# Kernel optimization log

Measured on AMD Instinct MI355X. Metric: run time of the kernel, lower is better.

The kernel has to match this reference:

```python
import jax, jax.numpy as jnp
import numpy as np

B, L, D = 8, 4096, 4096
E, R, K = 8, 16, 2
ALPHA = 1.0
EPS = 1e-5

def setup_inputs() -> dict:
    key = jax.random.key(0)
    ks = jax.random.split(key, 5)
    x = jax.random.normal(ks[0], (B, L, D), dtype=jnp.float32)
    gate_w = jax.random.normal(ks[1], (E, D), dtype=jnp.float32) * 0.02
    gate_b = jnp.zeros((E,), dtype=jnp.float32)
    A_w = jax.random.normal(ks[2], (E, R, D), dtype=jnp.float32) * 0.02
    B_w = jax.random.normal(ks[3], (E, D, R), dtype=jnp.float32) * 0.02
    gamma = jnp.ones((D,), dtype=jnp.float32)
    beta = jnp.zeros((D,), dtype=jnp.float32)
    return {"x": x, "gate_w": gate_w, "gate_b": gate_b, "A_w": A_w,
            "B_w": B_w, "gamma": gamma, "beta": beta}

def reference(x, gate_w, gate_b, A_w, B_w, gamma, beta):
    scale = ALPHA / R
    # pooled hidden state per sequence: [B, D]
    h = x.mean(axis=1)
    # router: gate logits -> top-k -> softmax over selected
    logits = h @ gate_w.T + gate_b                     # [B, E]
    top_vals, top_idx = jax.lax.top_k(logits, K)       # [B, K]
    w = jax.nn.softmax(top_vals, axis=-1)              # [B, K]
    # gather selected experts' LoRA factors
    A_sel = A_w[top_idx]                               # [B, K, R, D]
    B_sel = B_w[top_idx]                               # [B, K, D, R]
    z = jnp.einsum('bkrd,bd->bkr', A_sel, h)           # down-proj
    eo = jnp.einsum('bkdr,bkr->bkd', B_sel, z) * scale # up-proj
    delta = jnp.sum(w[..., None] * eo, axis=1)         # [B, D]
    # residual + LayerNorm (broadcast delta over seq dim)
    y = x + delta[:, None, :]
    mu = y.mean(axis=-1, keepdims=True)
    var = y.var(axis=-1, keepdims=True)
    return (y - mu) * jax.lax.rsqrt(var + EPS) * gamma + beta
```

## Files before the change

### kernel.cpp

```cpp
#include <hip/hip_runtime.h>

#define BB    8
#define LSEQ  4096
#define DD    4096
#define EE    8
#define RR    16
#define KK    2
#define NSLICE 128
#define LORA_SCALE (1.0f / 16.0f)
#define LN_EPS 1e-5f

typedef float f4 __attribute__((ext_vector_type(4)));

__device__ __forceinline__ float wave_sum(float v) {
#pragma unroll
    for (int off = 32; off > 0; off >>= 1)
        v += __shfl_xor(v, off, 64);
    return v;
}

__device__ __forceinline__ float dot4(f4 a, f4 b) {
    return a.x * b.x + a.y * b.y + a.z * b.z + a.w * b.w;
}

__global__ __launch_bounds__(256) void colsum_kernel(
    const f4* __restrict__ x, f4* __restrict__ partial, int rows_per_slice)
{
    const int tid = threadIdx.x;
    const int bid = blockIdx.x;
    const int b  = bid >> 7;
    const int sl = bid & (NSLICE - 1);
    const f4* p = x + ((size_t)b * LSEQ + (size_t)sl * rows_per_slice) * (DD / 4);

    f4 acc[4];
#pragma unroll
    for (int i = 0; i < 4; ++i) acc[i] = (f4)(0.f);

#pragma unroll 2
    for (int l = 0; l < rows_per_slice; ++l) {
        const f4* pr = p + (size_t)l * (DD / 4);
#pragma unroll
        for (int i = 0; i < 4; ++i)
            acc[i] += __builtin_nontemporal_load(&pr[tid + i * 256]);
    }
    f4* dst = partial + ((size_t)sl * BB + b) * (DD / 4);
#pragma unroll
    for (int i = 0; i < 4; ++i) dst[tid + i * 256] = acc[i];
}

__global__ __launch_bounds__(1024) void router_delta_kernel(
    const f4* __restrict__ partial, int nslice,
    const f4* __restrict__ gate_w, const float* __restrict__ gate_b,
    const f4* __restrict__ A_w, const f4* __restrict__ B_w,
    f4* __restrict__ delta)
{
    __shared__ float redl[EE * 16];
    __shared__ float lgbuf[EE];
    __shared__ float redz[KK * RR * 16];
    __shared__ float zbuf[KK * RR];
    __shared__ int   sel[KK];
    __shared__ float wsel[KK];

    const int b = blockIdx.x;
    const int tid = threadIdx.x;
    const int lane = tid & 63;
    const int wid = tid >> 6;

    f4 acc = (f4)(0.f);
#pragma unroll 8
    for (int sl = 0; sl < nslice; ++sl)
        acc += partial[((size_t)sl * BB + b) * (DD / 4) + tid];
    const f4 h = acc * (1.0f / LSEQ);

#pragma unroll
    for (int e = 0; e < EE; ++e) {
        float s = wave_sum(dot4(h, gate_w[e * (DD / 4) + tid]));
        if (lane == 0) redl[e * 16 + wid] = s;
    }
    __syncthreads();
    if (tid < EE) {
        float s = 0.f;
#pragma unroll
        for (int w = 0; w < 16; ++w) s += redl[tid * 16 + w];
        lgbuf[tid] = s + gate_b[tid];
    }
    __syncthreads();
    if (tid == 0) {
        int i0 = 0;
        for (int e = 1; e < EE; ++e) if (lgbuf[e] > lgbuf[i0]) i0 = e;
        int i1 = (i0 == 0) ? 1 : 0;
        for (int e = 0; e < EE; ++e) if (e != i0 && lgbuf[e] > lgbuf[i1]) i1 = e;
        float e1 = __expf(lgbuf[i1] - lgbuf[i0]);
        float inv = 1.0f / (1.0f + e1);
        sel[0] = i0; sel[1] = i1;
        wsel[0] = inv; wsel[1] = e1 * inv;
    }
    __syncthreads();

    const f4* A0 = A_w + (size_t)sel[0] * RR * (DD / 4);
    const f4* A1 = A_w + (size_t)sel[1] * RR * (DD / 4);
#pragma unroll
    for (int r = 0; r < RR; ++r) {
        float s0 = wave_sum(dot4(h, A0[r * (DD / 4) + tid]));
        float s1 = wave_sum(dot4(h, A1[r * (DD / 4) + tid]));
        if (lane == 0) {
            redz[r * 16 + wid] = s0;
            redz[(RR + r) * 16 + wid] = s1;
        }
    }
    __syncthreads();
    if (tid < KK * RR) {
        float s = 0.f;
#pragma unroll
        for (int w = 0; w < 16; ++w) s += redz[tid * 16 + w];
        zbuf[tid] = s;
    }
    __syncthreads();

    const float w0 = wsel[0], w1 = wsel[1];
    const f4* B0 = B_w + (size_t)sel[0] * DD * (RR / 4);
    const f4* B1 = B_w + (size_t)sel[1] * DD * (RR / 4);
    f4 o;
#pragma unroll
    for (int c = 0; c < 4; ++c) {
        const int d = tid * 4 + c;
        float s0 = 0.f, s1 = 0.f;
#pragma unroll
        for (int rv = 0; rv < RR / 4; ++rv) {
            f4 b0 = B0[d * (RR / 4) + rv];
            f4 b1 = B1[d * (RR / 4) + rv];
            s0 += b0.x * zbuf[rv * 4] + b0.y * zbuf[rv * 4 + 1]
                + b0.z * zbuf[rv * 4 + 2] + b0.w * zbuf[rv * 4 + 3];
            s1 += b1.x * zbuf[RR + rv * 4] + b1.y * zbuf[RR + rv * 4 + 1]
                + b1.z * zbuf[RR + rv * 4 + 2] + b1.w * zbuf[RR + rv * 4 + 3];
        }
        float v = LORA_SCALE * (w0 * s0 + w1 * s1);
        if (c == 0) o.x = v; else if (c == 1) o.y = v; else if (c == 2) o.z = v; else o.w = v;
    }
    delta[(size_t)b * (DD / 4) + tid] = o;
}

__global__ __launch_bounds__(256, 8) void resid_ln_kernel3(
    const f4* __restrict__ x, const f4* __restrict__ delta,
    const f4* __restrict__ gamma, const f4* __restrict__ beta,
    f4* __restrict__ out)
{
    __shared__ float red[4][2];
    const int tid = threadIdx.x;
    const int lane = tid & 63, w = tid >> 6;
    const int rp = (int)(gridDim.x - 1 - blockIdx.x);
    const size_t row = (size_t)rp * 2 + (w >> 1);
    const int half = w & 1;
    const int b = (int)(row >> 12);
    const int base = half * 512;
    const f4* xr = x + row * (DD / 4) + base;
    const f4* dr = delta + (size_t)b * (DD / 4) + base;

    f4 v[8];
    float sum = 0.f, sq = 0.f;
#pragma unroll
    for (int i = 0; i < 8; ++i) {
        const int idx = lane + i * 64;
        f4 xv = __builtin_nontemporal_load(&xr[idx]);
        xv += dr[idx];
        v[i] = xv;
        sum += xv.x + xv.y + xv.z + xv.w;
        sq  += xv.x * xv.x + xv.y * xv.y + xv.z * xv.z + xv.w * xv.w;
    }
    sum = wave_sum(sum);
    sq  = wave_sum(sq);
    if (lane == 0) { red[w][0] = sum; red[w][1] = sq; }
    __syncthreads();
    const float S = sum + red[w ^ 1][0];
    const float Q = sq  + red[w ^ 1][1];
    const float mean = S * (1.0f / DD);
    const float var  = Q * (1.0f / DD) - mean * mean;
    const float rstd = rsqrtf(var + LN_EPS);

    const f4* gr = gamma + base;
    const f4* br = beta + base;
    f4* orow = out + row * (DD / 4) + base;
#pragma unroll
    for (int i = 0; i < 8; ++i) {
        const int idx = lane + i * 64;
        f4 gv = gr[idx];
        f4 bv = br[idx];
        f4 xv = v[i];
        f4 o;
        o.x = (xv.x - mean) * rstd * gv.x + bv.x;
        o.y = (xv.y - mean) * rstd * gv.y + bv.y;
        o.z = (xv.z - mean) * rstd * gv.z + bv.z;
        o.w = (xv.w - mean) * rstd * gv.w + bv.w;
        __builtin_nontemporal_store(o, &orow[idx]);
    }
}

extern "C" void kernel_launch(void* const* d_in, const int* in_sizes, int n_in,
                              void* d_out, int out_size, void* d_ws, size_t ws_size,
                              hipStream_t stream) {
    const f4* x       = (const f4*)d_in[0];
    const f4* gate_w  = (const f4*)d_in[1];
    const float* gate_b = (const float*)d_in[2];
    const f4* A_w     = (const f4*)d_in[3];
    const f4* B_w     = (const f4*)d_in[4];
    const f4* gamma   = (const f4*)d_in[5];
    const f4* beta    = (const f4*)d_in[6];
    f4* out = (f4*)d_out;
    float* ws = (float*)d_ws;

    f4* partial = (f4*)ws;
    f4* delta   = (f4*)(ws + (size_t)NSLICE * BB * DD);

    colsum_kernel<<<BB * NSLICE, 256, 0, stream>>>(
        x, partial, LSEQ / NSLICE);

    router_delta_kernel<<<BB, 1024, 0, stream>>>(
        partial, NSLICE, gate_w, gate_b, A_w, B_w, delta);

    resid_ln_kernel3<<<BB * LSEQ / 2, 256, 0, stream>>>(
        x, delta, gamma, beta, out);
}
```

Measured before the change: 349.9 us.

## Process four rows per LayerNorm block to reuse delta, gamma and beta loads

The residual+LayerNorm kernel now handles four rows per 256-thread block. Each wave owns a quarter of the columns across all four rows, so delta, gamma and beta are loaded once and reused four times. All x loads are issued up front for more memory-level parallelism. The cost is higher register pressure (16 f4 values of x plus cached vectors), and the occupancy hint of 8 blocks per SM is dropped, which may lower occupancy.

```diff
diff --git a/kernel.cpp b/kernel.cpp
--- a/kernel.cpp
+++ b/kernel.cpp
@@ -140,58 +140,74 @@
     delta[(size_t)b * (DD / 4) + tid] = o;
 }
 
-__global__ __launch_bounds__(256, 8) void resid_ln_kernel3(
+__global__ __launch_bounds__(256) void resid_ln_kernel4(
     const f4* __restrict__ x, const f4* __restrict__ delta,
     const f4* __restrict__ gamma, const f4* __restrict__ beta,
     f4* __restrict__ out)
 {
-    __shared__ float red[4][2];
+    __shared__ float redS[4][4], redQ[4][4];
     const int tid = threadIdx.x;
     const int lane = tid & 63, w = tid >> 6;
     const int rp = (int)(gridDim.x - 1 - blockIdx.x);
-    const size_t row = (size_t)rp * 2 + (w >> 1);
-    const int half = w & 1;
-    const int b = (int)(row >> 12);
-    const int base = half * 512;
-    const f4* xr = x + row * (DD / 4) + base;
-    const f4* dr = delta + (size_t)b * (DD / 4) + base;
-
-    f4 v[8];
-    float sum = 0.f, sq = 0.f;
-#pragma unroll
-    for (int i = 0; i < 8; ++i) {
-        const int idx = lane + i * 64;
-        f4 xv = __builtin_nontemporal_load(&xr[idx]);
-        xv += dr[idx];
-        v[i] = xv;
-        sum += xv.x + xv.y + xv.z + xv.w;
-        sq  += xv.x * xv.x + xv.y * xv.y + xv.z * xv.z + xv.w * xv.w;
-    }
-    sum = wave_sum(sum);
-    sq  = wave_sum(sq);
-    if (lane == 0) { red[w][0] = sum; red[w][1] = sq; }
-    __syncthreads();
-    const float S = sum + red[w ^ 1][0];
-    const float Q = sq  + red[w ^ 1][1];
-    const float mean = S * (1.0f / DD);
-    const float var  = Q * (1.0f / DD) - mean * mean;
-    const float rstd = rsqrtf(var + LN_EPS);
-
-    const f4* gr = gamma + base;
-    const f4* br = beta + base;
-    f4* orow = out + row * (DD / 4) + base;
-#pragma unroll
-    for (int i = 0; i < 8; ++i) {
-        const int idx = lane + i * 64;
-        f4 gv = gr[idx];
-        f4 bv = br[idx];
-        f4 xv = v[i];
-        f4 o;
-        o.x = (xv.x - mean) * rstd * gv.x + bv.x;
-        o.y = (xv.y - mean) * rstd * gv.y + bv.y;
-        o.z = (xv.z - mean) * rstd * gv.z + bv.z;
-        o.w = (xv.w - mean) * rstd * gv.w + bv.w;
-        __builtin_nontemporal_store(o, &orow[idx]);
+    const size_t row0 = (size_t)rp * 4;
+    const int b = (int)(row0 >> 12);
+    const int qbase = w * 256;
+    const f4* dr = delta + (size_t)b * (DD / 4) + qbase;
+    const f4* gr = gamma + qbase;
+    const f4* br = beta + qbase;
+
+    f4 dv[4], gv[4], bv[4];
+#pragma unroll
+    for (int j = 0; j < 4; ++j) {
+        const int idx = lane + j * 64;
+        dv[j] = dr[idx];
+        gv[j] = gr[idx];
+        bv[j] = br[idx];
+    }
+
+    f4 v[4][4];
+#pragma unroll
+    for (int r = 0; r < 4; ++r) {
+        const f4* xr = x + (row0 + r) * (DD / 4) + qbase;
+#pragma unroll
+        for (int j = 0; j < 4; ++j)
+            v[r][j] = __builtin_nontemporal_load(&xr[lane + j * 64]);
+    }
+
+#pragma unroll
+    for (int r = 0; r < 4; ++r) {
+        float s = 0.f, q = 0.f;
+#pragma unroll
+        for (int j = 0; j < 4; ++j) {
+            f4 xv = v[r][j] + dv[j];
+            v[r][j] = xv;
+            s += xv.x + xv.y + xv.z + xv.w;
+            q += xv.x * xv.x + xv.y * xv.y + xv.z * xv.z + xv.w * xv.w;
+        }
+        s = wave_sum(s);
+        q = wave_sum(q);
+        if (lane == 0) { redS[r][w] = s; redQ[r][w] = q; }
+    }
+    __syncthreads();
+
+#pragma unroll
+    for (int r = 0; r < 4; ++r) {
+        const float S = redS[r][0] + redS[r][1] + redS[r][2] + redS[r][3];
+        const float Q = redQ[r][0] + redQ[r][1] + redQ[r][2] + redQ[r][3];
+        const float mean = S * (1.0f / DD);
+        const float var  = Q * (1.0f / DD) - mean * mean;
+        const float rstd = rsqrtf(var + LN_EPS);
+        f4* orow = out + (row0 + r) * (DD / 4) + qbase;
+#pragma unroll
+        for (int j = 0; j < 4; ++j) {
+            f4 xv = v[r][j];
+            f4 o;
+            o.x = (xv.x - mean) * rstd * gv[j].x + bv[j].x;
+            o.y = (xv.y - mean) * rstd * gv[j].y + bv[j].y;
+            o.z = (xv.z - mean) * rstd * gv[j].z + bv[j].z;
+            o.w = (xv.w - mean) * rstd * gv[j].w + bv[j].w;
+            __builtin_nontemporal_store(o, &orow[lane + j * 64]);
+        }
     }
 }
 
@@ -217,6 +233,6 @@
     router_delta_kernel<<<BB, 1024, 0, stream>>>(
         partial, NSLICE, gate_w, gate_b, A_w, B_w, delta);
 
-    resid_ln_kernel3<<<BB * LSEQ / 2, 256, 0, stream>>>(
+    resid_ln_kernel4<<<BB * LSEQ / 4, 256, 0, stream>>>(
         x, delta, gamma, beta, out);
 }
```

Result: faster. 323.1 us (-7.7%).
